# Kernel optimization log

Hardware: AMD Instinct MI355X
Metric: run time of the kernel (lower is better)

The kernel has to match this reference:

```python
import jax, jax.numpy as jnp
import numpy as np

B, N, C, D = 4, 4096, 1024, 32  # batch, tokens, channels, head dim
EPS = 1e-15
PAD_VAL = 1.0


def setup_inputs() -> dict:
    key = jax.random.key(0)
    k1, k2, k3 = jax.random.split(key, 3)
    x = jax.random.normal(k1, (B, N, C), dtype=jnp.float32)
    W_qkv = jax.random.normal(k2, (3 * C, C), dtype=jnp.float32) * 0.02
    W_proj = jax.random.normal(k3, (C, C), dtype=jnp.float32) * 0.02
    b_proj = jnp.zeros((C,), dtype=jnp.float32)
    return {"x": x, "W_qkv": W_qkv, "W_proj": W_proj, "b_proj": b_proj}


def reference(x, W_qkv, W_proj, b_proj):
    Bx, Nx, Cx = x.shape
    h = Cx // D
    # qkv projection (no bias), then split as torch: reshape(B,N,3,C).permute(0,2,3,1)
    qkv = jnp.einsum('bnc,oc->bno', x, W_qkv)            # [B,N,3C]
    qkv = qkv.reshape(Bx, Nx, 3, Cx).transpose(0, 2, 3, 1)  # [B,3,C,N]
    q, k, v = qkv[:, 0], qkv[:, 1], qkv[:, 2]
    q = jax.nn.relu(q.reshape(Bx, h, D, Nx))             # [B,h,D,N]
    k = jax.nn.relu(k.reshape(Bx, h, D, Nx)).transpose(0, 1, 3, 2)  # [B,h,N,D]
    v = v.reshape(Bx, h, D, Nx)                          # [B,h,D,N]
    # pad v with a row of PAD_VAL=1 to carry the normalizer
    v = jnp.concatenate([v, jnp.full((Bx, h, 1, Nx), PAD_VAL, v.dtype)], axis=2)  # [B,h,D+1,N]
    vk = jnp.einsum('bhdn,bhne->bhde', v, k)             # [B,h,D+1,D]
    out = jnp.einsum('bhde,bhen->bhdn', vk, q)           # [B,h,D+1,N]
    out = out[:, :, :-1] / (out[:, :, -1:] + EPS)        # [B,h,D,N]
    out = out.reshape(Bx, Cx, Nx).transpose(0, 2, 1)     # [B,N,C]
    return jnp.einsum('bnc,oc->bno', out, W_proj) + b_proj
```

## Files before the change

### kernel.cpp

```cpp
#include <hip/hip_runtime.h>


using us8   = __attribute__((ext_vector_type(8))) unsigned short;
using us4   = __attribute__((ext_vector_type(4))) unsigned short;
using s8v   = __attribute__((ext_vector_type(8))) short;
using f32x4 = __attribute__((ext_vector_type(4))) float;

__device__ __forceinline__ unsigned short f2bf(float f) {
    union { float f; unsigned int u; } c; c.f = f;
    unsigned int r = c.u + 0x7fffu + ((c.u >> 16) & 1u);
    return (unsigned short)(r >> 16);
}
__device__ __forceinline__ float bf2f(unsigned short u) {
    union { unsigned int u; float f; } c; c.u = ((unsigned int)u) << 16;
    return c.f;
}

__device__ __forceinline__ void async16(const unsigned short* g, unsigned short* l) {
    __builtin_amdgcn_global_load_lds(
        (const __attribute__((address_space(1))) unsigned int*)g,
        (__attribute__((address_space(3))) unsigned int*)l, 16, 0, 0);
}

__global__ __launch_bounds__(256)
void prep(const float* __restrict__ x, const float* __restrict__ wq,
          const float* __restrict__ wp, unsigned short* __restrict__ xb,
          unsigned short* __restrict__ wqb, unsigned short* __restrict__ wpb,
          float* __restrict__ vkws) {
    const int NX = 16777216 / 8, NQ = 3145728 / 8, NP = 1048576 / 8, NZ = 135168 / 8;
    int gid = blockIdx.x * 256 + threadIdx.x;
    const float* in; unsigned short* out; int i;
    if (gid < NX)                    { in = x;  out = xb;  i = gid * 8; }
    else if (gid < NX + NQ)          { in = wq; out = wqb; i = (gid - NX) * 8; }
    else if (gid < NX + NQ + NP)     { in = wp; out = wpb; i = (gid - NX - NQ) * 8; }
    else if (gid < NX + NQ + NP + NZ) {
        int z = (gid - NX - NQ - NP) * 8;
        f32x4 zero = {};
        *(f32x4*)(vkws + z) = zero; *(f32x4*)(vkws + z + 4) = zero;
        return;
    } else return;
    float4 a = *(const float4*)(in + i);
    float4 b = *(const float4*)(in + i + 4);
    us8 o;
    o[0] = f2bf(a.x); o[1] = f2bf(a.y); o[2] = f2bf(a.z); o[3] = f2bf(a.w);
    o[4] = f2bf(b.x); o[5] = f2bf(b.y); o[6] = f2bf(b.z); o[7] = f2bf(b.w);
    *(us8*)(out + i) = o;
}

template <int MODE>
__device__ __forceinline__
void gemm_core(const unsigned short* __restrict__ A,
               const unsigned short* __restrict__ Bt,
               void* __restrict__ C, unsigned short* __restrict__ kvT,
               const float* __restrict__ bias,
               int M, int N, int K, int tM, int tN) {
    __shared__ unsigned short As0[128 * 32], As1[128 * 32];
    __shared__ unsigned short Bs0[128 * 32], Bs1[128 * 32];

    const int tid  = threadIdx.x;
    const int lane = tid & 63;
    const int wv   = tid >> 6;
    const int wr   = wv >> 1, wc = wv & 1;

    f32x4 acc[4][4] = {};

    const int sseg = ((lane & 3) ^ ((lane >> 3) & 3)) * 8;
    const unsigned short* Ag = A + (size_t)(tM + wv * 32 + (lane >> 2)) * K + sseg;
    const unsigned short* Bg = Bt + (size_t)(tN + wv * 32 + (lane >> 2)) * K + sseg;
    const int wo = wv * 32 * 32;

    const int mrow = lane & 15;
    const int kqx  = (((lane >> 4) ^ ((lane >> 1) & 3))) * 8;

    for (int k0 = 0; k0 < K; k0 += 64) {
        __syncthreads();
        async16(Ag + k0,               &As0[wo]);
        async16(Ag + k0 + 16 * K,      &As0[wo + 16 * 32]);
        async16(Ag + k0 + 32,          &As1[wo]);
        async16(Ag + k0 + 32 + 16 * K, &As1[wo + 16 * 32]);
        async16(Bg + k0,               &Bs0[wo]);
        async16(Bg + k0 + 16 * K,      &Bs0[wo + 16 * 32]);
        async16(Bg + k0 + 32,          &Bs1[wo]);
        async16(Bg + k0 + 32 + 16 * K, &Bs1[wo + 16 * 32]);
        asm volatile("s_waitcnt vmcnt(0)" ::: "memory");
        __syncthreads();
        s8v af[4], bf[4];
#pragma unroll
        for (int mi = 0; mi < 4; ++mi)
            af[mi] = *(const s8v*)&As0[(wr * 64 + mi * 16 + mrow) * 32 + kqx];
#pragma unroll
        for (int ni = 0; ni < 4; ++ni)
            bf[ni] = *(const s8v*)&Bs0[(wc * 64 + ni * 16 + mrow) * 32 + kqx];
#pragma unroll
        for (int mi = 0; mi < 4; ++mi)
#pragma unroll
            for (int ni = 0; ni < 4; ++ni)
                acc[mi][ni] = __builtin_amdgcn_mfma_f32_16x16x32_bf16(
                    af[mi], bf[ni], acc[mi][ni], 0, 0, 0);
#pragma unroll
        for (int mi = 0; mi < 4; ++mi)
            af[mi] = *(const s8v*)&As1[(wr * 64 + mi * 16 + mrow) * 32 + kqx];
#pragma unroll
        for (int ni = 0; ni < 4; ++ni)
            bf[ni] = *(const s8v*)&Bs1[(wc * 64 + ni * 16 + mrow) * 32 + kqx];
#pragma unroll
        for (int mi = 0; mi < 4; ++mi)
#pragma unroll
            for (int ni = 0; ni < 4; ++ni)
                acc[mi][ni] = __builtin_amdgcn_mfma_f32_16x16x32_bf16(
                    af[mi], bf[ni], acc[mi][ni], 0, 0, 0);
    }

    const int crow0 = (lane >> 4) * 4;
    const int ccol  = lane & 15;
    if (MODE == 0 && tN >= 1024) {
        const int b2 = tM >> 12;
        const int nb0 = (tM & 4095) + wr * 64;
#pragma unroll
        for (int mi = 0; mi < 4; ++mi) {
            int nbase = nb0 + mi * 16 + crow0;
#pragma unroll
            for (int ni = 0; ni < 4; ++ni) {
                int col = tN + wc * 64 + ni * 16 + ccol;
                f32x4 v = acc[mi][ni];
                if (col < 2048) {
                    v[0] = fmaxf(v[0], 0.f); v[1] = fmaxf(v[1], 0.f);
                    v[2] = fmaxf(v[2], 0.f); v[3] = fmaxf(v[3], 0.f);
                }
                us4 o;
                o[0] = f2bf(v[0]); o[1] = f2bf(v[1]);
                o[2] = f2bf(v[2]); o[3] = f2bf(v[3]);
                *(us4*)&kvT[((size_t)b2 * 2048 + (col - 1024)) * 4096 + nbase] = o;
            }
        }
    } else {
#pragma unroll
        for (int mi = 0; mi < 4; ++mi)
#pragma unroll
            for (int ni = 0; ni < 4; ++ni) {
                int row = tM + wr * 64 + mi * 16 + crow0;
                int col = tN + wc * 64 + ni * 16 + ccol;
#pragma unroll
                for (int r2 = 0; r2 < 4; ++r2) {
                    float v = acc[mi][ni][r2];
                    if (MODE == 0) {
                        v = fmaxf(v, 0.f);
                        ((unsigned short*)C)[(size_t)(row + r2) * 1024 + col] = f2bf(v);
                    } else {
                        ((float*)C)[(size_t)(row + r2) * N + col] = v + bias[col];
                    }
                }
            }
    }
}

__device__ __forceinline__ void xcd_map(int blk, int MT, int& tM, int& tN) {
    const int xcd = blk & 7;
    const int i   = blk >> 3;
    const int MTx = MT >> 3;
    const int ppan = MTx * 8;
    const int p   = i / ppan;
    const int i2  = i % ppan;
    tM = (xcd * MTx + (i2 >> 3)) * 128;
    tN = (p * 8 + (i2 & 7)) * 128;
}

__global__ __launch_bounds__(256)
void gemm_qkv(const unsigned short* __restrict__ A,
              const unsigned short* __restrict__ Bt,
              unsigned short* __restrict__ Cq, unsigned short* __restrict__ kvT,
              int M, int N, int K) {
    int tM, tN;
    xcd_map(blockIdx.x, M >> 7, tM, tN);
    gemm_core<0>(A, Bt, (void*)Cq, kvT, nullptr, M, N, K, tM, tN);
}

__global__ __launch_bounds__(256)
void gemm_proj(const unsigned short* __restrict__ A,
               const unsigned short* __restrict__ Bt,
               float* __restrict__ C, const float* __restrict__ bias,
               int M, int N, int K) {
    int tM, tN;
    xcd_map(blockIdx.x, M >> 7, tM, tN);
    gemm_core<1>(A, Bt, (void*)C, nullptr, bias, M, N, K, tM, tN);
}

__global__ __launch_bounds__(256)
void lite_vk(const unsigned short* __restrict__ kvT, float* __restrict__ vkws) {
    const int bh = blockIdx.x, ck = blockIdx.y;
    const int b = bh >> 5, h = bh & 31;
    const int S = 136;
    __shared__ unsigned short Ks[32 * S];
    __shared__ unsigned short Vs[32 * S];
    __shared__ float Rs[4][1088];
    const int t = threadIdx.x, lane = t & 63, wv = t >> 6;
    const unsigned short* Kp = kvT + ((size_t)b * 2048 + h * 32) * 4096 + ck * 512;
    const unsigned short* Vp = kvT + ((size_t)b * 2048 + 1024 + h * 32) * 4096 + ck * 512;
    const int sr = t >> 3, ss = (t & 7) * 16;
    f32x4 acc00 = {}, acc01 = {}, acc10 = {}, acc11 = {}, accO0 = {}, accO1 = {};
    s8v ones;
#pragma unroll
    for (int j = 0; j < 8; ++j) ones[j] = (short)0x3F80;
    const int mrow = lane & 15, kq = (lane >> 4) * 8;

    for (int tile = 0; tile < 4; ++tile) {
        int go = tile * 128 + ss;
        us8 k0v = *(const us8*)(Kp + (size_t)sr * 4096 + go);
        us8 k1v = *(const us8*)(Kp + (size_t)sr * 4096 + go + 8);
        us8 v0v = *(const us8*)(Vp + (size_t)sr * 4096 + go);
        us8 v1v = *(const us8*)(Vp + (size_t)sr * 4096 + go + 8);
        __syncthreads();
        *(us8*)&Ks[sr * S + ss]     = k0v;
        *(us8*)&Ks[sr * S + ss + 8] = k1v;
        *(us8*)&Vs[sr * S + ss]     = v0v;
        *(us8*)&Vs[sr * S + ss + 8] = v1v;
        __syncthreads();
        int ko = wv * 32 + kq;
        s8v a0 = *(const s8v*)&Vs[(mrow)      * S + ko];
        s8v a1 = *(const s8v*)&Vs[(16 + mrow) * S + ko];
        s8v b0 = *(const s8v*)&Ks[(mrow)      * S + ko];
        s8v b1 = *(const s8v*)&Ks[(16 + mrow) * S + ko];
        acc00 = __builtin_amdgcn_mfma_f32_16x16x32_bf16(a0, b0, acc00, 0, 0, 0);
        acc01 = __builtin_amdgcn_mfma_f32_16x16x32_bf16(a0, b1, acc01, 0, 0, 0);
        acc10 = __builtin_amdgcn_mfma_f32_16x16x32_bf16(a1, b0, acc10, 0, 0, 0);
        acc11 = __builtin_amdgcn_mfma_f32_16x16x32_bf16(a1, b1, acc11, 0, 0, 0);
        accO0 = __builtin_amdgcn_mfma_f32_16x16x32_bf16(ones, b0, accO0, 0, 0, 0);
        accO1 = __builtin_amdgcn_mfma_f32_16x16x32_bf16(ones, b1, accO1, 0, 0, 0);
    }

    const int ccol = lane & 15, crow = (lane >> 4) * 4;
    float* R = Rs[wv];
#pragma unroll
    for (int r2 = 0; r2 < 4; ++r2) {
        R[(crow + r2) * 32 + ccol]           = acc00[r2];
        R[(crow + r2) * 32 + 16 + ccol]      = acc01[r2];
        R[(16 + crow + r2) * 32 + ccol]      = acc10[r2];
        R[(16 + crow + r2) * 32 + 16 + ccol] = acc11[r2];
    }
    if ((lane >> 4) == 0) {
        R[1024 + ccol]      = accO0[0];
        R[1024 + 16 + ccol] = accO1[0];
    }
    __syncthreads();
    float* vkb = vkws + bh * (33 * 32);
    for (int i = t; i < 1056; i += 256) {
        float s = Rs[0][i] + Rs[1][i] + Rs[2][i] + Rs[3][i];
        atomicAdd(&vkb[i], s);
    }
}

__global__ __launch_bounds__(256)
void lite_apply(const unsigned short* __restrict__ qb,
                const float* __restrict__ vkws,
                unsigned short* __restrict__ yb) {
    const int bh = blockIdx.x, nb = blockIdx.y;
    const int b = bh >> 5, h = bh & 31;
    __shared__ unsigned short vkh[48 * 32];
    __shared__ unsigned short vkl[48 * 32];
    const int t = threadIdx.x;
    for (int i = t; i < 48 * 32; i += 256) {
        float v = (i < 33 * 32) ? vkws[bh * (33 * 32) + i] : 0.f;
        unsigned short hi = f2bf(v);
        vkh[i] = hi;
        vkl[i] = f2bf(v - bf2f(hi));
    }
    __syncthreads();

    const int lane = t & 63, wv = t >> 6;
    const int col = lane & 15, quad = lane >> 4;
    s8v b0h = *(const s8v*)&vkh[(col)      * 32 + quad * 8];
    s8v b0l = *(const s8v*)&vkl[(col)      * 32 + quad * 8];
    s8v b1h = *(const s8v*)&vkh[(16 + col) * 32 + quad * 8];
    s8v b1l = *(const s8v*)&vkl[(16 + col) * 32 + quad * 8];
    s8v b2h = *(const s8v*)&vkh[(32 + col) * 32 + quad * 8];
    s8v b2l = *(const s8v*)&vkl[(32 + col) * 32 + quad * 8];

    const int ntile = nb * 256 + wv * 64;
#pragma unroll
    for (int mi = 0; mi < 4; ++mi) {
        int tok = ntile + mi * 16 + col;
        const unsigned short* qp =
            qb + (size_t)(b * 4096 + tok) * 1024 + h * 32 + quad * 8;
        s8v a = *(const s8v*)qp;
        f32x4 n0 = {}, n1 = {}, dd = {};
        n0 = __builtin_amdgcn_mfma_f32_16x16x32_bf16(b0h, a, n0, 0, 0, 0);
        n0 = __builtin_amdgcn_mfma_f32_16x16x32_bf16(b0l, a, n0, 0, 0, 0);
        n1 = __builtin_amdgcn_mfma_f32_16x16x32_bf16(b1h, a, n1, 0, 0, 0);
        n1 = __builtin_amdgcn_mfma_f32_16x16x32_bf16(b1l, a, n1, 0, 0, 0);
        dd = __builtin_amdgcn_mfma_f32_16x16x32_bf16(b2h, a, dd, 0, 0, 0);
        dd = __builtin_amdgcn_mfma_f32_16x16x32_bf16(b2l, a, dd, 0, 0, 0);
        float den  = __shfl(dd[0], col, 64);
        float rinv = 1.f / (den + 1e-15f);
        us4 o0, o1;
#pragma unroll
        for (int r = 0; r < 4; ++r) {
            o0[r] = f2bf(n0[r] * rinv);
            o1[r] = f2bf(n1[r] * rinv);
        }
        size_t o = (size_t)(b * 4096 + tok) * 1024 + h * 32;
        *(us4*)&yb[o + quad * 4]      = o0;
        *(us4*)&yb[o + 16 + quad * 4] = o1;
    }
}

extern "C" void kernel_launch(void* const* d_in, const int* in_sizes, int n_in,
                              void* d_out, int out_size, void* d_ws, size_t ws_size,
                              hipStream_t stream) {
    const float* x     = (const float*)d_in[0];
    const float* Wqkv  = (const float*)d_in[1];
    const float* Wproj = (const float*)d_in[2];
    const float* bproj = (const float*)d_in[3];
    float* out = (float*)d_out;

    const int M = 16384, Cdim = 1024, O1 = 3072;

    unsigned short* xb     = (unsigned short*)d_ws;
    unsigned short* wqkvb  = xb + (size_t)M * Cdim;
    unsigned short* wprojb = wqkvb + (size_t)O1 * Cdim;
    unsigned short* qb     = wprojb + (size_t)Cdim * Cdim;
    unsigned short* kvT    = qb + (size_t)M * Cdim;
    unsigned short* ybuf   = kvT + (size_t)4 * 2048 * 4096;
    float* vkws            = (float*)(ybuf + (size_t)M * Cdim);

    const int PREP_GROUPS = (16777216 + 3145728 + 1048576 + 135168) / 8;
    prep<<<(PREP_GROUPS + 255) / 256, 256, 0, stream>>>(
        x, Wqkv, Wproj, xb, wqkvb, wprojb, vkws);

    gemm_qkv<<<(M / 128) * (O1 / 128), 256, 0, stream>>>(
        xb, wqkvb, qb, kvT, M, O1, Cdim);

    lite_vk<<<dim3(128, 8), 256, 0, stream>>>(kvT, vkws);
    lite_apply<<<dim3(128, 16), 256, 0, stream>>>(qb, vkws, ybuf);

    gemm_proj<<<(M / 128) * (Cdim / 128), 256, 0, stream>>>(
        ybuf, wprojb, out, bproj, M, Cdim, Cdim);
}
```

Measured before the change: 333.3 us.

## Rewrite GEMMs as 256x256 tiles with multi-stage async LDS pipeline

Both projection GEMMs move from 128x128 tiles with a single-stage load-then-compute loop to 256x256 tiles run by 512 threads. The new loop uses 128 KB of dynamic LDS with double-buffered half-tiles, prefetching two k-steps ahead and interleaving async global-to-LDS loads with MFMA quads under raised wave priority. It also uses a deeper XOR swizzle and a new XCD tile mapping. The aim is to hide global load latency and raise data reuse per tile, at the cost of more registers and LDS per block, which lowers occupancy and leaves fewer blocks for the grid.

```diff
diff --git a/kernel.cpp b/kernel.cpp
--- a/kernel.cpp
+++ b/kernel.cpp
@@ -47,142 +47,208 @@
     *(us8*)(out + i) = o;
 }
 
+constexpr int HSZ = 128 * 64;
+
+#define FENCE() asm volatile("" ::: "memory")
+#define BARX()  do { FENCE(); __builtin_amdgcn_s_barrier(); FENCE(); } while (0)
+#define LGKM0() asm volatile("s_waitcnt lgkmcnt(0)" ::: "memory")
+
+#define MFMA_QUAD(MB, NB)                                                    \
+  do {                                                                       \
+    __builtin_amdgcn_s_setprio(1);                                           \
+    _Pragma("unroll")                                                        \
+    for (int mi_ = 0; mi_ < 4; ++mi_)                                        \
+      _Pragma("unroll")                                                      \
+      for (int ni_ = 0; ni_ < 2; ++ni_)                                      \
+        _Pragma("unroll")                                                    \
+        for (int kk_ = 0; kk_ < 2; ++kk_)                                    \
+          acc[(MB) + mi_][(NB) + ni_] =                                      \
+              __builtin_amdgcn_mfma_f32_16x16x32_bf16(                       \
+                  af[mi_][kk_], bf[(NB) + ni_][kk_],                         \
+                  acc[(MB) + mi_][(NB) + ni_], 0, 0, 0);                     \
+    __builtin_amdgcn_s_setprio(0);                                           \
+  } while (0)
+
+__device__ __forceinline__
+void stage_half(const unsigned short* __restrict__ G, int rowBase, int kcol,
+                unsigned short* ldsHalf, int row0, int esw, int wv) {
+    async16(G + (size_t)(rowBase + row0) * 1024 + kcol + esw,
+            ldsHalf + wv * 512);
+    async16(G + (size_t)(rowBase + 64 + row0) * 1024 + kcol + esw,
+            ldsHalf + 4096 + wv * 512);
+}
+
 template <int MODE>
 __device__ __forceinline__
-void gemm_core(const unsigned short* __restrict__ A,
-               const unsigned short* __restrict__ Bt,
-               void* __restrict__ C, unsigned short* __restrict__ kvT,
-               const float* __restrict__ bias,
-               int M, int N, int K, int tM, int tN) {
-    __shared__ unsigned short As0[128 * 32], As1[128 * 32];
-    __shared__ unsigned short Bs0[128 * 32], Bs1[128 * 32];
-
-    const int tid  = threadIdx.x;
-    const int lane = tid & 63;
-    const int wv   = tid >> 6;
-    const int wr   = wv >> 1, wc = wv & 1;
-
-    f32x4 acc[4][4] = {};
-
-    const int sseg = ((lane & 3) ^ ((lane >> 3) & 3)) * 8;
-    const unsigned short* Ag = A + (size_t)(tM + wv * 32 + (lane >> 2)) * K + sseg;
-    const unsigned short* Bg = Bt + (size_t)(tN + wv * 32 + (lane >> 2)) * K + sseg;
-    const int wo = wv * 32 * 32;
-
+void gemm_core256(const unsigned short* __restrict__ A,
+                  const unsigned short* __restrict__ Bt,
+                  unsigned short* __restrict__ Cq,
+                  unsigned short* __restrict__ kvT,
+                  float* __restrict__ Cf, const float* __restrict__ bias,
+                  int N, int tM, int tN, unsigned short* lds) {
+    unsigned short* As = lds;
+    unsigned short* Bs = lds + 4 * HSZ;
+
+    const int t    = threadIdx.x;
+    const int lane = t & 63;
+    const int wv   = t >> 6;
+    const int wr   = wv >> 2;
+    const int wc   = wv & 3;
     const int mrow = lane & 15;
-    const int kqx  = (((lane >> 4) ^ ((lane >> 1) & 3))) * 8;
-
-    for (int k0 = 0; k0 < K; k0 += 64) {
-        __syncthreads();
-        async16(Ag + k0,               &As0[wo]);
-        async16(Ag + k0 + 16 * K,      &As0[wo + 16 * 32]);
-        async16(Ag + k0 + 32,          &As1[wo]);
-        async16(Ag + k0 + 32 + 16 * K, &As1[wo + 16 * 32]);
-        async16(Bg + k0,               &Bs0[wo]);
-        async16(Bg + k0 + 16 * K,      &Bs0[wo + 16 * 32]);
-        async16(Bg + k0 + 32,          &Bs1[wo]);
-        async16(Bg + k0 + 32 + 16 * K, &Bs1[wo + 16 * 32]);
-        asm volatile("s_waitcnt vmcnt(0)" ::: "memory");
-        __syncthreads();
-        s8v af[4], bf[4];
-#pragma unroll
-        for (int mi = 0; mi < 4; ++mi)
-            af[mi] = *(const s8v*)&As0[(wr * 64 + mi * 16 + mrow) * 32 + kqx];
-#pragma unroll
-        for (int ni = 0; ni < 4; ++ni)
-            bf[ni] = *(const s8v*)&Bs0[(wc * 64 + ni * 16 + mrow) * 32 + kqx];
-#pragma unroll
-        for (int mi = 0; mi < 4; ++mi)
-#pragma unroll
-            for (int ni = 0; ni < 4; ++ni)
-                acc[mi][ni] = __builtin_amdgcn_mfma_f32_16x16x32_bf16(
-                    af[mi], bf[ni], acc[mi][ni], 0, 0, 0);
-#pragma unroll
-        for (int mi = 0; mi < 4; ++mi)
-            af[mi] = *(const s8v*)&As1[(wr * 64 + mi * 16 + mrow) * 32 + kqx];
-#pragma unroll
-        for (int ni = 0; ni < 4; ++ni)
-            bf[ni] = *(const s8v*)&Bs1[(wc * 64 + ni * 16 + mrow) * 32 + kqx];
-#pragma unroll
-        for (int mi = 0; mi < 4; ++mi)
-#pragma unroll
-            for (int ni = 0; ni < 4; ++ni)
-                acc[mi][ni] = __builtin_amdgcn_mfma_f32_16x16x32_bf16(
-                    af[mi], bf[ni], acc[mi][ni], 0, 0, 0);
-    }
-
-    const int crow0 = (lane >> 4) * 4;
-    const int ccol  = lane & 15;
-    if (MODE == 0 && tN >= 1024) {
-        const int b2 = tM >> 12;
-        const int nb0 = (tM & 4095) + wr * 64;
+    const int kq   = lane >> 4;
+    const int m7   = lane & 7;
+
+    const int row0 = t >> 3;
+    const int esw  = ((t & 7) ^ (row0 & 7)) * 8;
+
+    const int ks0 = ((0 * 4 + kq) ^ m7) * 8;
+    const int ks1 = ((1 * 4 + kq) ^ m7) * 8;
+    const int brow = (wc & 1) * 64;
+
+    f32x4 acc[8][4] = {};
+    s8v af[4][2], bf[4][2];
+
+    constexpr int NT = 16;
+
+    stage_half(A,  tM,       0,  As + 0 * HSZ, row0, esw, wv);
+    stage_half(A,  tM + 128, 0,  As + 1 * HSZ, row0, esw, wv);
+    stage_half(Bt, tN,       0,  Bs + 0 * HSZ, row0, esw, wv);
+    stage_half(Bt, tN + 128, 0,  Bs + 1 * HSZ, row0, esw, wv);
+    stage_half(Bt, tN,       64, Bs + 2 * HSZ, row0, esw, wv);
+    stage_half(Bt, tN + 128, 64, Bs + 3 * HSZ, row0, esw, wv);
+    stage_half(A,  tM,       64, As + 2 * HSZ, row0, esw, wv);
+    asm volatile("s_waitcnt vmcnt(6)" ::: "memory");
+    BARX();
+
+    for (int g = 0; g < NT; ++g) {
+        const int c = g & 1;
+        const unsigned short* Ard = As + (c * 2 + wr) * HSZ;
+        const unsigned short* Brd = Bs + (c * 2 + (wc >> 1)) * HSZ;
+        const int kt1 = (g + 1 < NT ? g + 1 : NT - 1) * 64;
+        const int kt2 = (g + 2 < NT ? g + 2 : NT - 1) * 64;
+
+#pragma unroll
+        for (int ni = 0; ni < 2; ++ni) {
+            bf[ni][0] = *(const s8v*)&Brd[(brow + ni * 16 + mrow) * 64 + ks0];
+            bf[ni][1] = *(const s8v*)&Brd[(brow + ni * 16 + mrow) * 64 + ks1];
+        }
 #pragma unroll
         for (int mi = 0; mi < 4; ++mi) {
-            int nbase = nb0 + mi * 16 + crow0;
-#pragma unroll
-            for (int ni = 0; ni < 4; ++ni) {
-                int col = tN + wc * 64 + ni * 16 + ccol;
-                f32x4 v = acc[mi][ni];
-                if (col < 2048) {
-                    v[0] = fmaxf(v[0], 0.f); v[1] = fmaxf(v[1], 0.f);
-                    v[2] = fmaxf(v[2], 0.f); v[3] = fmaxf(v[3], 0.f);
-                }
-                us4 o;
-                o[0] = f2bf(v[0]); o[1] = f2bf(v[1]);
-                o[2] = f2bf(v[2]); o[3] = f2bf(v[3]);
-                *(us4*)&kvT[((size_t)b2 * 2048 + (col - 1024)) * 4096 + nbase] = o;
-            }
-        }
-    } else {
-#pragma unroll
-        for (int mi = 0; mi < 4; ++mi)
-#pragma unroll
-            for (int ni = 0; ni < 4; ++ni) {
-                int row = tM + wr * 64 + mi * 16 + crow0;
-                int col = tN + wc * 64 + ni * 16 + ccol;
-#pragma unroll
-                for (int r2 = 0; r2 < 4; ++r2) {
-                    float v = acc[mi][ni][r2];
-                    if (MODE == 0) {
-                        v = fmaxf(v, 0.f);
-                        ((unsigned short*)C)[(size_t)(row + r2) * 1024 + col] = f2bf(v);
-                    } else {
-                        ((float*)C)[(size_t)(row + r2) * N + col] = v + bias[col];
+            af[mi][0] = *(const s8v*)&Ard[(mi * 16 + mrow) * 64 + ks0];
+            af[mi][1] = *(const s8v*)&Ard[(mi * 16 + mrow) * 64 + ks1];
+        }
+#pragma unroll
+        for (int ni = 2; ni < 4; ++ni) {
+            bf[ni][0] = *(const s8v*)&Brd[(brow + ni * 16 + mrow) * 64 + ks0];
+            bf[ni][1] = *(const s8v*)&Brd[(brow + ni * 16 + mrow) * 64 + ks1];
+        }
+        stage_half(A, tM + 128, kt1, As + ((c ^ 1) * 2 + 1) * HSZ, row0, esw, wv);
+        MFMA_QUAD(0, 0);
+        LGKM0();
+        BARX();
+
+        stage_half(Bt, tN, kt2, Bs + (c * 2 + 0) * HSZ, row0, esw, wv);
+        MFMA_QUAD(0, 2);
+        BARX();
+
+#pragma unroll
+        for (int mi = 0; mi < 4; ++mi) {
+            af[mi][0] = *(const s8v*)&Ard[(64 + mi * 16 + mrow) * 64 + ks0];
+            af[mi][1] = *(const s8v*)&Ard[(64 + mi * 16 + mrow) * 64 + ks1];
+        }
+        stage_half(Bt, tN + 128, kt2, Bs + (c * 2 + 1) * HSZ, row0, esw, wv);
+        MFMA_QUAD(4, 0);
+        LGKM0();
+        BARX();
+
+        stage_half(A, tM, kt2, As + (c * 2 + 0) * HSZ, row0, esw, wv);
+        MFMA_QUAD(4, 2);
+        asm volatile("s_waitcnt vmcnt(6)" ::: "memory");
+        BARX();
+    }
+
+    const int crow0 = kq * 4;
+    const int ccol  = mrow;
+    if (MODE == 0) {
+        if (tN >= 1024) {
+            const int b2  = tM >> 12;
+            const int nb0 = (tM & 4095) + wr * 128;
+#pragma unroll
+            for (int mi = 0; mi < 8; ++mi) {
+                const int nbase = nb0 + mi * 16 + crow0;
+#pragma unroll
+                for (int ni = 0; ni < 4; ++ni) {
+                    const int col = tN + wc * 64 + ni * 16 + ccol;
+                    f32x4 v = acc[mi][ni];
+                    if (col < 2048) {
+                        v[0] = fmaxf(v[0], 0.f); v[1] = fmaxf(v[1], 0.f);
+                        v[2] = fmaxf(v[2], 0.f); v[3] = fmaxf(v[3], 0.f);
                     }
+                    us4 o;
+                    o[0] = f2bf(v[0]); o[1] = f2bf(v[1]);
+                    o[2] = f2bf(v[2]); o[3] = f2bf(v[3]);
+                    *(us4*)&kvT[((size_t)b2 * 2048 + (col - 1024)) * 4096 + nbase] = o;
                 }
             }
-    }
-}
-
-__device__ __forceinline__ void xcd_map(int blk, int MT, int& tM, int& tN) {
+        } else {
+#pragma unroll
+            for (int mi = 0; mi < 8; ++mi)
+#pragma unroll
+                for (int ni = 0; ni < 4; ++ni) {
+                    const int row = tM + wr * 128 + mi * 16 + crow0;
+                    const int col = tN + wc * 64 + ni * 16 + ccol;
+#pragma unroll
+                    for (int r2 = 0; r2 < 4; ++r2)
+                        Cq[(size_t)(row + r2) * 1024 + col] =
+                            f2bf(fmaxf(acc[mi][ni][r2], 0.f));
+                }
+        }
+    } else {
+#pragma unroll
+        for (int mi = 0; mi < 8; ++mi)
+#pragma unroll
+            for (int ni = 0; ni < 4; ++ni) {
+                const int row = tM + wr * 128 + mi * 16 + crow0;
+                const int col = tN + wc * 64 + ni * 16 + ccol;
+#pragma unroll
+                for (int r2 = 0; r2 < 4; ++r2)
+                    Cf[(size_t)(row + r2) * N + col] = acc[mi][ni][r2] + bias[col];
+            }
+    }
+    asm volatile("s_waitcnt vmcnt(0)" ::: "memory");
+}
+
+__device__ __forceinline__ void xcd_map256(int blk, int MT, int& tM, int& tN) {
     const int xcd = blk & 7;
     const int i   = blk >> 3;
     const int MTx = MT >> 3;
-    const int ppan = MTx * 8;
+    const int ppan = MTx * 4;
     const int p   = i / ppan;
     const int i2  = i % ppan;
-    tM = (xcd * MTx + (i2 >> 3)) * 128;
-    tN = (p * 8 + (i2 & 7)) * 128;
-}
-
-__global__ __launch_bounds__(256)
+    tM = (xcd * MTx + (i2 >> 2)) * 256;
+    tN = (p * 4 + (i2 & 3)) * 256;
+}
+
+__global__ __launch_bounds__(512, 2)
 void gemm_qkv(const unsigned short* __restrict__ A,
               const unsigned short* __restrict__ Bt,
               unsigned short* __restrict__ Cq, unsigned short* __restrict__ kvT,
-              int M, int N, int K) {
+              int M, int N) {
+    extern __shared__ unsigned short lds[];
     int tM, tN;
-    xcd_map(blockIdx.x, M >> 7, tM, tN);
-    gemm_core<0>(A, Bt, (void*)Cq, kvT, nullptr, M, N, K, tM, tN);
-}
-
-__global__ __launch_bounds__(256)
+    xcd_map256(blockIdx.x, M >> 8, tM, tN);
+    gemm_core256<0>(A, Bt, Cq, kvT, nullptr, nullptr, N, tM, tN, lds);
+}
+
+__global__ __launch_bounds__(512, 2)
 void gemm_proj(const unsigned short* __restrict__ A,
                const unsigned short* __restrict__ Bt,
                float* __restrict__ C, const float* __restrict__ bias,
-               int M, int N, int K) {
+               int M, int N) {
+    extern __shared__ unsigned short lds[];
     int tM, tN;
-    xcd_map(blockIdx.x, M >> 7, tM, tN);
-    gemm_core<1>(A, Bt, (void*)C, nullptr, bias, M, N, K, tM, tN);
+    xcd_map256(blockIdx.x, M >> 8, tM, tN);
+    gemm_core256<1>(A, Bt, nullptr, nullptr, C, bias, N, tM, tN, lds);
 }
 
 __global__ __launch_bounds__(256)
@@ -322,16 +388,25 @@
     unsigned short* ybuf   = kvT + (size_t)4 * 2048 * 4096;
     float* vkws            = (float*)(ybuf + (size_t)M * Cdim);
 
+    static int attr_done = 0;
+    if (!attr_done) {
+        hipFuncSetAttribute((const void*)gemm_qkv,
+                            hipFuncAttributeMaxDynamicSharedMemorySize, 131072);
+        hipFuncSetAttribute((const void*)gemm_proj,
+                            hipFuncAttributeMaxDynamicSharedMemorySize, 131072);
+        attr_done = 1;
+    }
+
     const int PREP_GROUPS = (16777216 + 3145728 + 1048576 + 135168) / 8;
     prep<<<(PREP_GROUPS + 255) / 256, 256, 0, stream>>>(
         x, Wqkv, Wproj, xb, wqkvb, wprojb, vkws);
 
-    gemm_qkv<<<(M / 128) * (O1 / 128), 256, 0, stream>>>(
-        xb, wqkvb, qb, kvT, M, O1, Cdim);
+    gemm_qkv<<<(M / 256) * (O1 / 256), 512, 131072, stream>>>(
+        xb, wqkvb, qb, kvT, M, O1);
 
     lite_vk<<<dim3(128, 8), 256, 0, stream>>>(kvT, vkws);
     lite_apply<<<dim3(128, 16), 256, 0, stream>>>(qb, vkws, ybuf);
 
-    gemm_proj<<<(M / 128) * (Cdim / 128), 256, 0, stream>>>(
-        ybuf, wprojb, out, bproj, M, Cdim, Cdim);
-}
+    gemm_proj<<<(M / 256) * (Cdim / 256), 512, 131072, stream>>>(
+        ybuf, wprojb, out, bproj, M, Cdim);
+}
```

Measured after the change: 311.5 us. 6.5% less time.

## Pipeline GEMM mainloop with triple-buffered async LDS loads and new swizzle

Applied to the files above, without the earlier changes.

Rewrites the shared GEMM core used by the QKV and output projections. It uses a three-stage ring of 32-wide K tiles in dynamic LDS, prefetching two tiles ahead with global_load_lds so loads overlap the MFMA work. The old loop waited on all loads with two barriers per step. It also adds a new XOR swizzle for LDS, raises MFMA wave priority, requests 3 blocks per CU, and narrows the XCD panel mapping from 8 to 4 column tiles. The cost is more LDS per block (48KB) and a hard-coded K=1024 with fixed unroll, plus tighter vmcnt bookkeeping.

```diff
diff --git a/kernel.cpp b/kernel.cpp
--- a/kernel.cpp
+++ b/kernel.cpp
@@ -47,142 +47,165 @@
     *(us8*)(out + i) = o;
 }
 
+#define FENCE() asm volatile("" ::: "memory")
+#define BARX()  do { FENCE(); __builtin_amdgcn_s_barrier(); FENCE(); } while (0)
+
+__device__ __forceinline__ int sdec(int c) {
+    int line = c >> 3, slot = c & 7;
+    int sraw = slot ^ (line & 7);
+    return (line * 2 + (sraw >> 2)) * 1024 + (sraw & 3) * 8;
+}
+
 template <int MODE>
 __device__ __forceinline__
-void gemm_core(const unsigned short* __restrict__ A,
-               const unsigned short* __restrict__ Bt,
-               void* __restrict__ C, unsigned short* __restrict__ kvT,
-               const float* __restrict__ bias,
-               int M, int N, int K, int tM, int tN) {
-    __shared__ unsigned short As0[128 * 32], As1[128 * 32];
-    __shared__ unsigned short Bs0[128 * 32], Bs1[128 * 32];
-
-    const int tid  = threadIdx.x;
-    const int lane = tid & 63;
-    const int wv   = tid >> 6;
-    const int wr   = wv >> 1, wc = wv & 1;
+void gemm_core128(const unsigned short* __restrict__ A,
+                  const unsigned short* __restrict__ Bt,
+                  unsigned short* __restrict__ Cq,
+                  unsigned short* __restrict__ kvT,
+                  float* __restrict__ Cf, const float* __restrict__ bias,
+                  int N, int tM, int tN, unsigned short* lds) {
+    unsigned short* As = lds;
+    unsigned short* Bs = lds + 12288;
+
+    const int t    = threadIdx.x;
+    const int lane = t & 63;
+    const int wv   = t >> 6;
+    const int wr   = wv >> 1;
+    const int wc   = wv & 1;
+    const int mrow = lane & 15;
+    const int kq   = lane >> 4;
+
+    const int g0 = sdec(t), g1 = sdec(256 + t);
+    const unsigned short* Ag0 = A  + (size_t)tM * 1024 + g0;
+    const unsigned short* Ag1 = A  + (size_t)tM * 1024 + g1;
+    const unsigned short* Bg0 = Bt + (size_t)tN * 1024 + g0;
+    const unsigned short* Bg1 = Bt + (size_t)tN * 1024 + g1;
+    const int dst0 = wv * 512, dst1 = 2048 + wv * 512;
+
+    const int rA = wr * 64 + mrow, lA = rA >> 1;
+    const int aoff = lA * 64 + ((((rA & 1) << 2) | kq) ^ (lA & 7)) * 8;
+    const int rB = wc * 64 + mrow, lB = rB >> 1;
+    const int boff = lB * 64 + ((((rB & 1) << 2) | kq) ^ (lB & 7)) * 8;
 
     f32x4 acc[4][4] = {};
-
-    const int sseg = ((lane & 3) ^ ((lane >> 3) & 3)) * 8;
-    const unsigned short* Ag = A + (size_t)(tM + wv * 32 + (lane >> 2)) * K + sseg;
-    const unsigned short* Bg = Bt + (size_t)(tN + wv * 32 + (lane >> 2)) * K + sseg;
-    const int wo = wv * 32 * 32;
-
-    const int mrow = lane & 15;
-    const int kqx  = (((lane >> 4) ^ ((lane >> 1) & 3))) * 8;
-
-    for (int k0 = 0; k0 < K; k0 += 64) {
-        __syncthreads();
-        async16(Ag + k0,               &As0[wo]);
-        async16(Ag + k0 + 16 * K,      &As0[wo + 16 * 32]);
-        async16(Ag + k0 + 32,          &As1[wo]);
-        async16(Ag + k0 + 32 + 16 * K, &As1[wo + 16 * 32]);
-        async16(Bg + k0,               &Bs0[wo]);
-        async16(Bg + k0 + 16 * K,      &Bs0[wo + 16 * 32]);
-        async16(Bg + k0 + 32,          &Bs1[wo]);
-        async16(Bg + k0 + 32 + 16 * K, &Bs1[wo + 16 * 32]);
-        asm volatile("s_waitcnt vmcnt(0)" ::: "memory");
-        __syncthreads();
-        s8v af[4], bf[4];
+    s8v af[4], bf[4];
+
+    async16(Ag0, As + dst0);            async16(Ag1, As + dst1);
+    async16(Bg0, Bs + dst0);            async16(Bg1, Bs + dst1);
+    async16(Ag0 + 32, As + 4096 + dst0); async16(Ag1 + 32, As + 4096 + dst1);
+    async16(Bg0 + 32, Bs + 4096 + dst0); async16(Bg1 + 32, Bs + 4096 + dst1);
+    asm volatile("s_waitcnt vmcnt(4)" ::: "memory");
+    BARX();
+
+#pragma unroll
+    for (int g = 0; g < 32; ++g) {
+        const int rb = g % 3, sb = (g + 2) % 3;
+        const int kt = (g + 2 < 32 ? g + 2 : 31) * 32;
+        const unsigned short* Ar = As + rb * 4096;
+        const unsigned short* Br = Bs + rb * 4096;
 #pragma unroll
         for (int mi = 0; mi < 4; ++mi)
-            af[mi] = *(const s8v*)&As0[(wr * 64 + mi * 16 + mrow) * 32 + kqx];
+            af[mi] = *(const s8v*)&Ar[aoff + mi * 512];
 #pragma unroll
         for (int ni = 0; ni < 4; ++ni)
-            bf[ni] = *(const s8v*)&Bs0[(wc * 64 + ni * 16 + mrow) * 32 + kqx];
+            bf[ni] = *(const s8v*)&Br[boff + ni * 512];
+        async16(Ag0 + kt, As + sb * 4096 + dst0);
+        async16(Ag1 + kt, As + sb * 4096 + dst1);
+        async16(Bg0 + kt, Bs + sb * 4096 + dst0);
+        async16(Bg1 + kt, Bs + sb * 4096 + dst1);
+        __builtin_amdgcn_s_setprio(1);
 #pragma unroll
         for (int mi = 0; mi < 4; ++mi)
 #pragma unroll
             for (int ni = 0; ni < 4; ++ni)
                 acc[mi][ni] = __builtin_amdgcn_mfma_f32_16x16x32_bf16(
                     af[mi], bf[ni], acc[mi][ni], 0, 0, 0);
-#pragma unroll
-        for (int mi = 0; mi < 4; ++mi)
-            af[mi] = *(const s8v*)&As1[(wr * 64 + mi * 16 + mrow) * 32 + kqx];
-#pragma unroll
-        for (int ni = 0; ni < 4; ++ni)
-            bf[ni] = *(const s8v*)&Bs1[(wc * 64 + ni * 16 + mrow) * 32 + kqx];
-#pragma unroll
-        for (int mi = 0; mi < 4; ++mi)
-#pragma unroll
-            for (int ni = 0; ni < 4; ++ni)
-                acc[mi][ni] = __builtin_amdgcn_mfma_f32_16x16x32_bf16(
-                    af[mi], bf[ni], acc[mi][ni], 0, 0, 0);
-    }
-
-    const int crow0 = (lane >> 4) * 4;
-    const int ccol  = lane & 15;
-    if (MODE == 0 && tN >= 1024) {
-        const int b2 = tM >> 12;
-        const int nb0 = (tM & 4095) + wr * 64;
-#pragma unroll
-        for (int mi = 0; mi < 4; ++mi) {
-            int nbase = nb0 + mi * 16 + crow0;
-#pragma unroll
-            for (int ni = 0; ni < 4; ++ni) {
-                int col = tN + wc * 64 + ni * 16 + ccol;
-                f32x4 v = acc[mi][ni];
-                if (col < 2048) {
-                    v[0] = fmaxf(v[0], 0.f); v[1] = fmaxf(v[1], 0.f);
-                    v[2] = fmaxf(v[2], 0.f); v[3] = fmaxf(v[3], 0.f);
+        __builtin_amdgcn_s_setprio(0);
+        asm volatile("s_waitcnt vmcnt(4)" ::: "memory");
+        BARX();
+    }
+
+    const int crow0 = kq * 4;
+    if (MODE == 0) {
+        if (tN >= 1024) {
+            const int b2  = tM >> 12;
+            const int nb0 = (tM & 4095) + wr * 64;
+#pragma unroll
+            for (int mi = 0; mi < 4; ++mi) {
+                const int nbase = nb0 + mi * 16 + crow0;
+#pragma unroll
+                for (int ni = 0; ni < 4; ++ni) {
+                    const int col = tN + wc * 64 + ni * 16 + mrow;
+                    f32x4 v = acc[mi][ni];
+                    if (col < 2048) {
+                        v[0] = fmaxf(v[0], 0.f); v[1] = fmaxf(v[1], 0.f);
+                        v[2] = fmaxf(v[2], 0.f); v[3] = fmaxf(v[3], 0.f);
+                    }
+                    us4 o;
+                    o[0] = f2bf(v[0]); o[1] = f2bf(v[1]);
+                    o[2] = f2bf(v[2]); o[3] = f2bf(v[3]);
+                    *(us4*)&kvT[((size_t)b2 * 2048 + (col - 1024)) * 4096 + nbase] = o;
                 }
-                us4 o;
-                o[0] = f2bf(v[0]); o[1] = f2bf(v[1]);
-                o[2] = f2bf(v[2]); o[3] = f2bf(v[3]);
-                *(us4*)&kvT[((size_t)b2 * 2048 + (col - 1024)) * 4096 + nbase] = o;
             }
+        } else {
+#pragma unroll
+            for (int mi = 0; mi < 4; ++mi)
+#pragma unroll
+                for (int ni = 0; ni < 4; ++ni) {
+                    const int row = tM + wr * 64 + mi * 16 + crow0;
+                    const int col = tN + wc * 64 + ni * 16 + mrow;
+#pragma unroll
+                    for (int r2 = 0; r2 < 4; ++r2)
+                        Cq[(size_t)(row + r2) * 1024 + col] =
+                            f2bf(fmaxf(acc[mi][ni][r2], 0.f));
+                }
         }
     } else {
 #pragma unroll
         for (int mi = 0; mi < 4; ++mi)
 #pragma unroll
             for (int ni = 0; ni < 4; ++ni) {
-                int row = tM + wr * 64 + mi * 16 + crow0;
-                int col = tN + wc * 64 + ni * 16 + ccol;
-#pragma unroll
-                for (int r2 = 0; r2 < 4; ++r2) {
-                    float v = acc[mi][ni][r2];
-                    if (MODE == 0) {
-                        v = fmaxf(v, 0.f);
-                        ((unsigned short*)C)[(size_t)(row + r2) * 1024 + col] = f2bf(v);
-                    } else {
-                        ((float*)C)[(size_t)(row + r2) * N + col] = v + bias[col];
-                    }
-                }
+                const int row = tM + wr * 64 + mi * 16 + crow0;
+                const int col = tN + wc * 64 + ni * 16 + mrow;
+#pragma unroll
+                for (int r2 = 0; r2 < 4; ++r2)
+                    Cf[(size_t)(row + r2) * N + col] = acc[mi][ni][r2] + bias[col];
             }
     }
-}
-
-__device__ __forceinline__ void xcd_map(int blk, int MT, int& tM, int& tN) {
+    asm volatile("s_waitcnt vmcnt(0)" ::: "memory");
+}
+
+__device__ __forceinline__ void xcd_map128(int blk, int MT, int& tM, int& tN) {
     const int xcd = blk & 7;
     const int i   = blk >> 3;
     const int MTx = MT >> 3;
-    const int ppan = MTx * 8;
+    const int ppan = MTx * 4;
     const int p   = i / ppan;
     const int i2  = i % ppan;
-    tM = (xcd * MTx + (i2 >> 3)) * 128;
-    tN = (p * 8 + (i2 & 7)) * 128;
-}
-
-__global__ __launch_bounds__(256)
+    tM = (xcd * MTx + (i2 >> 2)) * 128;
+    tN = (p * 4 + (i2 & 3)) * 128;
+}
+
+__global__ __launch_bounds__(256, 3)
 void gemm_qkv(const unsigned short* __restrict__ A,
               const unsigned short* __restrict__ Bt,
               unsigned short* __restrict__ Cq, unsigned short* __restrict__ kvT,
-              int M, int N, int K) {
+              int M, int N) {
+    extern __shared__ unsigned short lds[];
     int tM, tN;
-    xcd_map(blockIdx.x, M >> 7, tM, tN);
-    gemm_core<0>(A, Bt, (void*)Cq, kvT, nullptr, M, N, K, tM, tN);
-}
-
-__global__ __launch_bounds__(256)
+    xcd_map128(blockIdx.x, M >> 7, tM, tN);
+    gemm_core128<0>(A, Bt, Cq, kvT, nullptr, nullptr, N, tM, tN, lds);
+}
+
+__global__ __launch_bounds__(256, 3)
 void gemm_proj(const unsigned short* __restrict__ A,
                const unsigned short* __restrict__ Bt,
                float* __restrict__ C, const float* __restrict__ bias,
-               int M, int N, int K) {
+               int M, int N) {
+    extern __shared__ unsigned short lds[];
     int tM, tN;
-    xcd_map(blockIdx.x, M >> 7, tM, tN);
-    gemm_core<1>(A, Bt, (void*)C, nullptr, bias, M, N, K, tM, tN);
+    xcd_map128(blockIdx.x, M >> 7, tM, tN);
+    gemm_core128<1>(A, Bt, nullptr, nullptr, C, bias, N, tM, tN, lds);
 }
 
 __global__ __launch_bounds__(256)
@@ -322,16 +345,25 @@
     unsigned short* ybuf   = kvT + (size_t)4 * 2048 * 4096;
     float* vkws            = (float*)(ybuf + (size_t)M * Cdim);
 
+    static int attr_done = 0;
+    if (!attr_done) {
+        hipFuncSetAttribute((const void*)gemm_qkv,
+                            hipFuncAttributeMaxDynamicSharedMemorySize, 49152);
+        hipFuncSetAttribute((const void*)gemm_proj,
+                            hipFuncAttributeMaxDynamicSharedMemorySize, 49152);
+        attr_done = 1;
+    }
+
     const int PREP_GROUPS = (16777216 + 3145728 + 1048576 + 135168) / 8;
     prep<<<(PREP_GROUPS + 255) / 256, 256, 0, stream>>>(
         x, Wqkv, Wproj, xb, wqkvb, wprojb, vkws);
 
-    gemm_qkv<<<(M / 128) * (O1 / 128), 256, 0, stream>>>(
-        xb, wqkvb, qb, kvT, M, O1, Cdim);
+    gemm_qkv<<<(M / 128) * (O1 / 128), 256, 49152, stream>>>(
+        xb, wqkvb, qb, kvT, M, O1);
 
     lite_vk<<<dim3(128, 8), 256, 0, stream>>>(kvT, vkws);
     lite_apply<<<dim3(128, 16), 256, 0, stream>>>(qb, vkws, ybuf);
 
-    gemm_proj<<<(M / 128) * (Cdim / 128), 256, 0, stream>>>(
-        ybuf, wprojb, out, bproj, M, Cdim, Cdim);
-}
+    gemm_proj<<<(M / 128) * (Cdim / 128), 256, 49152, stream>>>(
+        ybuf, wprojb, out, bproj, M, Cdim);
+}
```

Result: no change. 339.4 us (+1.8%).
